# Kernel tuning notes

Measured on AMD Instinct MI355X. Metric: run time of the kernel, lower is better.

The kernel has to match this reference:

```python
import jax, jax.numpy as jnp
import numpy as np

N, IN_CAPS, IN_LEN = 32, 1152, 32
OUT_CAPS, OUT_LEN = 64, 32
NUM_ITERATIONS = 3


def setup_inputs() -> dict:
    key = jax.random.key(0)
    k1, k2 = jax.random.split(key)
    x = jax.random.normal(k1, (N, IN_CAPS, IN_LEN), dtype=jnp.float32)
    # learnable weight, torch.randn init: (out_capsules, out_length, in_length)
    weight = jax.random.normal(k2, (OUT_CAPS, OUT_LEN, IN_LEN), dtype=jnp.float32)
    return {"x": x, "weight": weight}


def _squash(v):
    # v * ||v|| / (1 + ||v||^2)  ==  (||v||^2/(1+||v||^2)) * v/||v||
    norm_sq = jnp.sum(v * v, axis=-1, keepdims=True)
    norm = jnp.sqrt(norm_sq)
    return v * norm / (1.0 + norm_sq)


def reference(x, weight):
    # priors u_hat: [N, out_caps, in_caps, out_len]
    priors = jnp.einsum('oli,bni->bonl', weight, x)
    logits = jnp.zeros_like(priors)
    output = None
    for r in range(NUM_ITERATIONS):
        # coupling coefficients: softmax over output capsules (axis=1)
        probs = jax.nn.softmax(logits, axis=1)
        # weighted sum over input capsules -> [N, out_caps, 1, out_len]
        output = jnp.sum(probs * priors, axis=-2, keepdims=True)
        if r != NUM_ITERATIONS - 1:
            output = _squash(output)
            # agreement update: [N, out_caps, in_caps, 1]
            logits = logits + jnp.sum(priors * output, axis=-1, keepdims=True)
    output = _squash(output)  # squash=True default
    return jnp.squeeze(output, axis=-2)  # [N, out_caps, out_len]
```

## Files before the change

kernel.cpp:

```cpp
#include <hip/hip_runtime.h>
#include <math.h>


#define N_B      32
#define IN_CAPS  1152
#define IN_LEN   32
#define OUT_CAPS 64
#define OUT_LEN  32

#define NCHUNK 16
#define NPB    (IN_CAPS / NCHUNK)
#define PASS_WAVES 4
#define NPW    (NPB / PASS_WAVES)
#define TSTR   33
#define FSTR   36

#define DECODE_BC(d, b, c) \
    const int _slot = (d) >> 3; \
    const int b = ((d) & 7) * 4 + (_slot >> 4); \
    const int c = _slot & 15;

#define DPPV(v, ctrl) \
    __int_as_float(__builtin_amdgcn_update_dpp(0, __float_as_int(v), ctrl, 0xF, 0xF, true))

__device__ __forceinline__ float wave_max(float v) {
    v = fmaxf(v, DPPV(v, 0xB1));
    v = fmaxf(v, DPPV(v, 0x4E));
    v = fmaxf(v, DPPV(v, 0x141));
    v = fmaxf(v, DPPV(v, 0x140));
    v = fmaxf(v, __shfl_xor(v, 16, 64));
    v = fmaxf(v, __shfl_xor(v, 32, 64));
    return v;
}
__device__ __forceinline__ float wave_sum(float v) {
    v += DPPV(v, 0xB1);
    v += DPPV(v, 0x4E);
    v += DPPV(v, 0x141);
    v += DPPV(v, 0x140);
    v += __shfl_xor(v, 16, 64);
    v += __shfl_xor(v, 32, 64);
    return v;
}

__device__ __forceinline__ void pass_v2(const float* __restrict__ x,
                                        const float* t_lds,
                                        float* buf,
                                        float* __restrict__ part_out,
                                        int b, int c, int tid, int lane, int wave) {
    float s[IN_LEN];
#pragma unroll
    for (int i = 0; i < IN_LEN; ++i) s[i] = 0.f;

    const float* xw = x + ((size_t)b * IN_CAPS + c * NPB + wave * NPW) * IN_LEN;
    const float* tr = t_lds + lane * TSTR;

#define L4(acc, R, k) \
    acc = fmaf((R).x, tr[k],     acc); acc = fmaf((R).y, tr[k + 1], acc); \
    acc = fmaf((R).z, tr[k + 2], acc); acc = fmaf((R).w, tr[k + 3], acc);
#define S4(R, k) \
    s[k]     = fmaf(prob, (R).x, s[k]);     s[k + 1] = fmaf(prob, (R).y, s[k + 1]); \
    s[k + 2] = fmaf(prob, (R).z, s[k + 2]); s[k + 3] = fmaf(prob, (R).w, s[k + 3]);

#pragma unroll
    for (int j = 0; j < NPW; ++j) {
        const float4* xr = (const float4*)(xw + j * IN_LEN);
        const float4 r0 = xr[0], r1 = xr[1], r2 = xr[2], r3 = xr[3],
                     r4 = xr[4], r5 = xr[5], r6 = xr[6], r7 = xr[7];

        float l0 = 0.f, l1 = 0.f, l2 = 0.f, l3 = 0.f;
        L4(l0, r0, 0)  L4(l1, r1, 4)  L4(l2, r2, 8)  L4(l3, r3, 12)
        L4(l0, r4, 16) L4(l1, r5, 20) L4(l2, r6, 24) L4(l3, r7, 28)
        const float logit = (l0 + l1) + (l2 + l3);

        const float m = wave_max(logit);
        const float p = __expf(logit - m);
        const float S = wave_sum(p);
        const float prob = p * __builtin_amdgcn_rcpf(S);

        S4(r0, 0)  S4(r1, 4)  S4(r2, 8)  S4(r3, 12)
        S4(r4, 16) S4(r5, 20) S4(r6, 24) S4(r7, 28)
    }
#undef L4
#undef S4

    {
        float4* dst = (float4*)&buf[(wave * OUT_CAPS + lane) * FSTR];
#pragma unroll
        for (int q = 0; q < 8; ++q)
            dst[q] = make_float4(s[4 * q], s[4 * q + 1], s[4 * q + 2], s[4 * q + 3]);
    }
    __syncthreads();
    {
        float4* pb4 = (float4*)(part_out + ((size_t)b * NCHUNK + c) * OUT_CAPS * IN_LEN);
        for (int e = tid; e < OUT_CAPS * IN_LEN / 4; e += 256) {
            const int o = e >> 3, q4 = (e & 7) * 4;
            const float4 a0 = *(const float4*)&buf[(0 * OUT_CAPS + o) * FSTR + q4];
            const float4 a1 = *(const float4*)&buf[(1 * OUT_CAPS + o) * FSTR + q4];
            const float4 a2 = *(const float4*)&buf[(2 * OUT_CAPS + o) * FSTR + q4];
            const float4 a3 = *(const float4*)&buf[(3 * OUT_CAPS + o) * FSTR + q4];
            pb4[e] = make_float4(a0.x + a1.x + a2.x + a3.x,
                                 a0.y + a1.y + a2.y + a3.y,
                                 a0.z + a1.z + a2.z + a3.z,
                                 a0.w + a1.w + a2.w + a3.w);
        }
    }
}

__global__ __launch_bounds__(512) void k_init(const float* __restrict__ x,
                                              const float* __restrict__ W,
                                              float* __restrict__ T) {
    const int d   = blockIdx.x;
    const int b   = (d & 7) * 4 + (d >> 3);
    const int tid = threadIdx.x;
    const float* xb = x + (size_t)b * IN_CAPS * IN_LEN;

    __shared__ float4 red4[64][8];
    {
        const int q = tid & 7;
        const int g = tid >> 3;
        float4 acc = make_float4(0.f, 0.f, 0.f, 0.f);
        for (int n = g; n < IN_CAPS; n += 64) {
            const float4 v = *(const float4*)(xb + n * IN_LEN + q * 4);
            acc.x += v.x; acc.y += v.y; acc.z += v.z; acc.w += v.w;
        }
        red4[g][q] = acc;
    }
    __syncthreads();
    __shared__ float s0[IN_LEN];
    if (tid < 8) {
        float4 v = make_float4(0.f, 0.f, 0.f, 0.f);
#pragma unroll 16
        for (int g = 0; g < 64; ++g) {
            const float4 r = red4[g][tid];
            v.x += r.x; v.y += r.y; v.z += r.z; v.w += r.w;
        }
        const float inv = 1.f / 64.f;
        s0[tid * 4 + 0] = v.x * inv;
        s0[tid * 4 + 1] = v.y * inv;
        s0[tid * 4 + 2] = v.z * inv;
        s0[tid * 4 + 3] = v.w * inv;
    }
    __syncthreads();

    __shared__ float u[OUT_CAPS * OUT_LEN];
    for (int e = tid; e < OUT_CAPS * OUT_LEN; e += 512) {
        const float* wrow = W + (size_t)e * IN_LEN;
        float a = 0.f;
#pragma unroll
        for (int i = 0; i < IN_LEN; ++i) a = fmaf(wrow[i], s0[i], a);
        u[e] = a;
    }
    __syncthreads();

    __shared__ float scale[OUT_CAPS];
    if (tid < OUT_CAPS) {
        float ns = 0.f;
#pragma unroll
        for (int l = 0; l < OUT_LEN; ++l) { const float v = u[tid * OUT_LEN + l]; ns = fmaf(v, v, ns); }
        scale[tid] = sqrtf(ns) / (1.f + ns);
    }
    __syncthreads();

    for (int e = tid; e < OUT_CAPS * IN_LEN; e += 512) {
        const int o = e >> 5, i = e & 31;
        float a = 0.f;
#pragma unroll
        for (int l = 0; l < OUT_LEN; ++l)
            a = fmaf(W[((size_t)o * OUT_LEN + l) * IN_LEN + i], u[o * OUT_LEN + l], a);
        T[(size_t)b * OUT_CAPS * IN_LEN + e] = a * scale[o];
    }
}

__global__ __launch_bounds__(256, 2) void k_pass1(const float* __restrict__ x,
                                                  const float* __restrict__ T,
                                                  float* __restrict__ part) {
    DECODE_BC(blockIdx.x, b, c)
    const int tid  = threadIdx.x;
    const int lane = tid & 63;
    const int wave = __builtin_amdgcn_readfirstlane(tid >> 6);

    __shared__ float t_lds[OUT_CAPS * TSTR];
    __shared__ __align__(16) float buf[PASS_WAVES * OUT_CAPS * FSTR];

    {
        const float* Tb = T + (size_t)b * OUT_CAPS * IN_LEN;
        for (int e = tid; e < OUT_CAPS * IN_LEN; e += 256)
            t_lds[(e >> 5) * TSTR + (e & 31)] = Tb[e];
    }
    __syncthreads();

    pass_v2(x, t_lds, buf, part, b, c, tid, lane, wave);
}

__global__ __launch_bounds__(256, 2) void kB(const float* __restrict__ x,
                                             const float* __restrict__ W,
                                             const float* __restrict__ T,
                                             const float* __restrict__ part,
                                             float* __restrict__ part2) {
    DECODE_BC(blockIdx.x, b, c)
    const int tid  = threadIdx.x;
    const int lane = tid & 63;
    const int wave = __builtin_amdgcn_readfirstlane(tid >> 6);

    __shared__ float t_lds[OUT_CAPS * TSTR];
    __shared__ __align__(16) float buf[PASS_WAVES * OUT_CAPS * FSTR];

    float* uu = buf + 2048;
    float* sc = buf + 4096;

    {
        const float4* pb4 = (const float4*)(part + (size_t)b * NCHUNK * OUT_CAPS * IN_LEN);
        float4* wp = (float4*)buf + wave * 512;
        for (int e = lane; e < 512; e += 64) {
            float4 acc = make_float4(0.f, 0.f, 0.f, 0.f);
#pragma unroll
            for (int k = 0; k < 4; ++k) {
                const float4 v = pb4[(size_t)(wave + 4 * k) * 512 + e];
                acc.x += v.x; acc.y += v.y; acc.z += v.z; acc.w += v.w;
            }
            wp[e] = acc;
        }
    }
    __syncthreads();
    {
        float4* b4 = (float4*)buf;
        for (int e = tid; e < 512; e += 256) {
            const float4 a0 = b4[e], a1 = b4[512 + e], a2 = b4[1024 + e], a3 = b4[1536 + e];
            b4[e] = make_float4(a0.x + a1.x + a2.x + a3.x,
                                a0.y + a1.y + a2.y + a3.y,
                                a0.z + a1.z + a2.z + a3.z,
                                a0.w + a1.w + a2.w + a3.w);
        }
    }
    __syncthreads();

    for (int e = tid; e < OUT_CAPS * OUT_LEN; e += 256) {
        const int o = e >> 5;
        const float* wrow = W + (size_t)e * IN_LEN;
        const float* srow = buf + o * IN_LEN;
        float a = 0.f;
#pragma unroll
        for (int i = 0; i < IN_LEN; ++i) a = fmaf(wrow[i], srow[i], a);
        uu[e] = a;
    }
    __syncthreads();
    if (tid < OUT_CAPS) {
        float ns = 0.f;
#pragma unroll
        for (int l = 0; l < OUT_LEN; ++l) { const float v = uu[tid * OUT_LEN + l]; ns = fmaf(v, v, ns); }
        sc[tid] = sqrtf(ns) / (1.f + ns);
    }
    __syncthreads();

    for (int e = tid; e < OUT_CAPS * IN_LEN; e += 256) {
        const int o = e >> 5, i = e & 31;
        float a = 0.f;
#pragma unroll
        for (int l = 0; l < OUT_LEN; ++l)
            a = fmaf(W[((size_t)o * OUT_LEN + l) * IN_LEN + i], uu[o * OUT_LEN + l], a);
        t_lds[o * TSTR + i] = T[(size_t)b * OUT_CAPS * IN_LEN + e] + a * sc[o];
    }
    __syncthreads();

    pass_v2(x, t_lds, buf, part2, b, c, tid, lane, wave);
}

__global__ __launch_bounds__(256) void kC(const float* __restrict__ W,
                                          const float* __restrict__ part2,
                                          float* __restrict__ out) {
    const int d   = blockIdx.x;
    const int b   = (d & 7) * 4 + ((d >> 3) & 3);
    const int og  = d >> 5;
    const int tid = threadIdx.x;
    const int ol  = tid >> 5;
    const int i   = tid & 31;
    const int o   = og * 8 + ol;

    float a = 0.f;
    const float* pb = part2 + (size_t)b * NCHUNK * OUT_CAPS * IN_LEN + o * IN_LEN + i;
#pragma unroll
    for (int cc = 0; cc < NCHUNK; ++cc) a += pb[cc * OUT_CAPS * IN_LEN];

    __shared__ float s_lds[8][33];
    s_lds[ol][i] = a;
    __syncthreads();

    const float* wrow = W + ((size_t)o * OUT_LEN + i) * IN_LEN;
    float u = 0.f;
#pragma unroll
    for (int k = 0; k < IN_LEN; ++k) u = fmaf(wrow[k], s_lds[ol][k], u);

    float ns = u * u;
    ns += __shfl_xor(ns, 1, 64);
    ns += __shfl_xor(ns, 2, 64);
    ns += __shfl_xor(ns, 4, 64);
    ns += __shfl_xor(ns, 8, 64);
    ns += __shfl_xor(ns, 16, 64);
    const float scale = sqrtf(ns) / (1.f + ns);

    out[((size_t)b * OUT_CAPS + o) * OUT_LEN + i] = u * scale;
}

extern "C" void kernel_launch(void* const* d_in, const int* in_sizes, int n_in,
                              void* d_out, int out_size, void* d_ws, size_t ws_size,
                              hipStream_t stream) {
    const float* x = (const float*)d_in[0];
    const float* W = (const float*)d_in[1];
    float* out = (float*)d_out;

    float* T     = (float*)d_ws;
    float* part  = T + (size_t)N_B * OUT_CAPS * IN_LEN;
    float* part2 = part + (size_t)N_B * NCHUNK * OUT_CAPS * IN_LEN;

    k_init <<<N_B,          512, 0, stream>>>(x, W, T);
    k_pass1<<<N_B * NCHUNK, 256, 0, stream>>>(x, T, part);
    kB     <<<N_B * NCHUNK, 256, 0, stream>>>(x, W, T, part, part2);
    kC     <<<N_B * 8,      256, 0, stream>>>(W, part2, out);
}
```

Baseline: 120.6 us.

## Fuse init kernel into first routing pass, recomputing T per chunk block

Merges k_init into k_pass1 so each of the 512 (batch, chunk) blocks recomputes the per-batch mean of x, the u vector and the T matrix redundantly, writes it straight into LDS, and only chunk 0 stores T to global for later kernels. This removes one kernel launch and the global round trip of T between init and the first pass. In exchange every block re-reads the full x slice for its batch and all of W, which adds 16x redundant compute and memory traffic for the init stage. It also reuses the pass scratch buffer for the reduction scratch.

```diff
diff --git a/kernel.cpp b/kernel.cpp
--- a/kernel.cpp
+++ b/kernel.cpp
@@ -106,32 +106,39 @@
     }
 }
 
-__global__ __launch_bounds__(512) void k_init(const float* __restrict__ x,
-                                              const float* __restrict__ W,
-                                              float* __restrict__ T) {
-    const int d   = blockIdx.x;
-    const int b   = (d & 7) * 4 + (d >> 3);
-    const int tid = threadIdx.x;
+__global__ __launch_bounds__(256, 2) void kA(const float* __restrict__ x,
+                                             const float* __restrict__ W,
+                                             float* __restrict__ T,
+                                             float* __restrict__ part) {
+    DECODE_BC(blockIdx.x, b, c)
+    const int tid  = threadIdx.x;
+    const int lane = tid & 63;
+    const int wave = __builtin_amdgcn_readfirstlane(tid >> 6);
+
+    __shared__ float t_lds[OUT_CAPS * TSTR];
+    __shared__ __align__(16) float buf[PASS_WAVES * OUT_CAPS * FSTR];
+
     const float* xb = x + (size_t)b * IN_CAPS * IN_LEN;
 
-    __shared__ float4 red4[64][8];
-    {
-        const int q = tid & 7;
-        const int g = tid >> 3;
+    {
+        float4* red4 = (float4*)buf;
+        const int q = tid & 7, g = tid >> 3;
         float4 acc = make_float4(0.f, 0.f, 0.f, 0.f);
-        for (int n = g; n < IN_CAPS; n += 64) {
+        for (int n = g; n < IN_CAPS; n += 32) {
             const float4 v = *(const float4*)(xb + n * IN_LEN + q * 4);
             acc.x += v.x; acc.y += v.y; acc.z += v.z; acc.w += v.w;
         }
-        red4[g][q] = acc;
-    }
-    __syncthreads();
-    __shared__ float s0[IN_LEN];
+        red4[g * 8 + q] = acc;
+    }
+    __syncthreads();
+    float* u     = buf + 1024;
+    float* scale = buf + 3072;
+    float* s0    = buf + 3136;
     if (tid < 8) {
+        const float4* red4 = (const float4*)buf;
         float4 v = make_float4(0.f, 0.f, 0.f, 0.f);
-#pragma unroll 16
-        for (int g = 0; g < 64; ++g) {
-            const float4 r = red4[g][tid];
+        for (int g = 0; g < 32; ++g) {
+            const float4 r = red4[g * 8 + tid];
             v.x += r.x; v.y += r.y; v.z += r.z; v.w += r.w;
         }
         const float inv = 1.f / 64.f;
@@ -142,8 +149,7 @@
     }
     __syncthreads();
 
-    __shared__ float u[OUT_CAPS * OUT_LEN];
-    for (int e = tid; e < OUT_CAPS * OUT_LEN; e += 512) {
+    for (int e = tid; e < OUT_CAPS * OUT_LEN; e += 256) {
         const float* wrow = W + (size_t)e * IN_LEN;
         float a = 0.f;
 #pragma unroll
@@ -151,8 +157,6 @@
         u[e] = a;
     }
     __syncthreads();
-
-    __shared__ float scale[OUT_CAPS];
     if (tid < OUT_CAPS) {
         float ns = 0.f;
 #pragma unroll
@@ -161,31 +165,15 @@
     }
     __syncthreads();
 
-    for (int e = tid; e < OUT_CAPS * IN_LEN; e += 512) {
+    for (int e = tid; e < OUT_CAPS * IN_LEN; e += 256) {
         const int o = e >> 5, i = e & 31;
         float a = 0.f;
 #pragma unroll
         for (int l = 0; l < OUT_LEN; ++l)
             a = fmaf(W[((size_t)o * OUT_LEN + l) * IN_LEN + i], u[o * OUT_LEN + l], a);
-        T[(size_t)b * OUT_CAPS * IN_LEN + e] = a * scale[o];
-    }
-}
-
-__global__ __launch_bounds__(256, 2) void k_pass1(const float* __restrict__ x,
-                                                  const float* __restrict__ T,
-                                                  float* __restrict__ part) {
-    DECODE_BC(blockIdx.x, b, c)
-    const int tid  = threadIdx.x;
-    const int lane = tid & 63;
-    const int wave = __builtin_amdgcn_readfirstlane(tid >> 6);
-
-    __shared__ float t_lds[OUT_CAPS * TSTR];
-    __shared__ __align__(16) float buf[PASS_WAVES * OUT_CAPS * FSTR];
-
-    {
-        const float* Tb = T + (size_t)b * OUT_CAPS * IN_LEN;
-        for (int e = tid; e < OUT_CAPS * IN_LEN; e += 256)
-            t_lds[(e >> 5) * TSTR + (e & 31)] = Tb[e];
+        const float val = a * scale[o];
+        t_lds[o * TSTR + i] = val;
+        if (c == 0) T[(size_t)b * OUT_CAPS * IN_LEN + e] = val;
     }
     __syncthreads();
 
@@ -312,8 +300,7 @@
     float* part  = T + (size_t)N_B * OUT_CAPS * IN_LEN;
     float* part2 = part + (size_t)N_B * NCHUNK * OUT_CAPS * IN_LEN;
 
-    k_init <<<N_B,          512, 0, stream>>>(x, W, T);
-    k_pass1<<<N_B * NCHUNK, 256, 0, stream>>>(x, T, part);
-    kB     <<<N_B * NCHUNK, 256, 0, stream>>>(x, W, T, part, part2);
-    kC     <<<N_B * 8,      256, 0, stream>>>(W, part2, out);
-}
+    kA<<<N_B * NCHUNK, 256, 0, stream>>>(x, W, T, part);
+    kB<<<N_B * NCHUNK, 256, 0, stream>>>(x, W, T, part, part2);
+    kC<<<N_B * 8,      256, 0, stream>>>(W, part2, out);
+}
```

New measurement: 129.7 us. +7.5%, slower.
